# Performance work log

Hardware: AMD Instinct MI355X
Metric: run time of the kernel (lower is better)

Reference implementation:

```python
import jax, jax.numpy as jnp
import numpy as np

B, D, T, H, E = 4, 1024, 2048, 16, 64  # batch, dim, seq_len, n_heads, hidden_dim (H*E == D)


def setup_inputs() -> dict:
    key = jax.random.key(0)
    ks = jax.random.split(key, 6)
    x = jax.random.normal(ks[0], (B, D, T), dtype=jnp.float32)            # (b, e, t) layout
    Wp = jax.random.normal(ks[1], (H, E, D), dtype=jnp.float32) / np.sqrt(D)  # per-head proj weights
    bp = jax.random.normal(ks[2], (H, E), dtype=jnp.float32) * 0.01
    tw = jax.random.normal(ks[3], (H, T), dtype=jnp.float32) / np.sqrt(T)  # per-head Toeplitz kernel, tw[h,0]=diagonal
    Wo = jax.random.normal(ks[4], (D, D), dtype=jnp.float32) / np.sqrt(D)
    bo = jax.random.normal(ks[5], (D,), dtype=jnp.float32) * 0.01
    return {"x": x, "Wp": Wp, "bp": bp, "tw": tw, "Wo": Wo, "bo": bo}


def reference(x, Wp, bp, tw, Wo, bo):
    # x: (b, dim, t) -> (b, t, dim)
    xt = jnp.transpose(x, (0, 2, 1))
    # per-head projections: (b, h, e, t)
    proj = jnp.einsum('btd,hed->bhet', xt, Wp) + bp[None, :, :, None]
    # build per-head causal lower-triangular Toeplitz matrices: Tm[h, t, s] = tw[h, t-s] if s <= t else 0
    idx = jnp.arange(T)[:, None] - jnp.arange(T)[None, :]  # (t, s)
    Tm = jnp.where(idx >= 0, tw[:, jnp.clip(idx, 0)], 0.0)  # (h, t, s)
    # causal Toeplitz mixing along time per head
    mixed = jnp.einsum('hts,bhes->bhet', Tm, proj)          # (b, h, e, t)
    # concat heads on feature dim: (b, t, h*e) == (b, t, dim)
    cat = jnp.transpose(mixed, (0, 3, 1, 2)).reshape(B, T, H * E)
    out = cat @ Wo.T + bo                                   # out_proj: Linear(dim, dim)
    return jnp.transpose(out, (0, 2, 1))                    # back to (b, e, t)
```

## Files before the change

kernel.cpp:

```cpp
#include <hip/hip_runtime.h>
#include <cstdint>

#define NB 4
#define ND 1024
#define NT 2048
#define NH 16
#define NE 64
#define GLEN 2240
#define CAP 2312

typedef __bf16 bf16x8 __attribute__((ext_vector_type(8)));
typedef float f32x4 __attribute__((ext_vector_type(4)));
typedef unsigned short us8 __attribute__((ext_vector_type(8)));
typedef unsigned short us4 __attribute__((ext_vector_type(4)));

__device__ __forceinline__ unsigned short f2bf(float f) {
  unsigned u = __builtin_bit_cast(unsigned, f);
  return (unsigned short)((u + 0x7fffu + ((u >> 16) & 1u)) >> 16);
}

__device__ __forceinline__ void gload16(const void* g, void* l) {
  __builtin_amdgcn_global_load_lds(
      (const __attribute__((address_space(1))) void*)(uintptr_t)g,
      (__attribute__((address_space(3))) void*)(uintptr_t)l, 16, 0, 0);
}

__global__ void prep_kernel(const float* __restrict__ Wp, const float* __restrict__ Wo,
                            const float* __restrict__ tw,
                            unsigned short* __restrict__ WpB, unsigned short* __restrict__ WoB,
                            unsigned short* __restrict__ Gr8) {
  int idx = blockIdx.x * 256 + threadIdx.x;
  int stride = gridDim.x * 256;
  const int n4 = ND * ND / 4;
  for (int i = idx; i < n4; i += stride) {
    float4 v = ((const float4*)Wp)[i];
    us4 o = {f2bf(v.x), f2bf(v.y), f2bf(v.z), f2bf(v.w)};
    ((us4*)WpB)[i] = o;
  }
  for (int i = idx; i < n4; i += stride) {
    float4 v = ((const float4*)Wo)[i];
    us4 o = {f2bf(v.x), f2bf(v.y), f2bf(v.z), f2bf(v.w)};
    ((us4*)WoB)[i] = o;
  }
  for (int i = idx; i < NH * 8 * GLEN; i += stride) {
    int h = i / (8 * GLEN);
    int rem = i - h * 8 * GLEN;
    int r = rem / GLEN;
    int c = rem - r * GLEN;
    int src = c + r;
    Gr8[i] = (src <= NT - 1) ? f2bf(tw[h * NT + (NT - 1) - src]) : (unsigned short)0;
  }
}

__global__ __launch_bounds__(256) void transpose_cast(const float* __restrict__ x,
                                                      unsigned short* __restrict__ xT) {
  __shared__ float tile[64][65];
  const int c = threadIdx.x & 15, r = threadIdx.x >> 4;
  const int t0 = blockIdx.x * 64, d0 = blockIdx.y * 64, b = blockIdx.z;
  const float* xb = x + (long)b * ND * NT;
#pragma unroll
  for (int k = 0; k < 4; ++k) {
    float4 v = *(const float4*)&xb[(long)(d0 + r + 16 * k) * NT + t0 + 4 * c];
    tile[r + 16 * k][4 * c + 0] = v.x;
    tile[r + 16 * k][4 * c + 1] = v.y;
    tile[r + 16 * k][4 * c + 2] = v.z;
    tile[r + 16 * k][4 * c + 3] = v.w;
  }
  __syncthreads();
  unsigned short* xTb = xT + (long)b * NT * ND;
#pragma unroll
  for (int k = 0; k < 4; ++k) {
    int t = r + 16 * k;
    us4 o = {f2bf(tile[4 * c + 0][t]), f2bf(tile[4 * c + 1][t]), f2bf(tile[4 * c + 2][t]),
             f2bf(tile[4 * c + 3][t])};
    *(us4*)&xTb[(long)(t0 + t) * ND + d0 + 4 * c] = o;
  }
}

template <bool OUT_BF16>
__global__ __launch_bounds__(512, 2) void gemm_bt(const unsigned short* __restrict__ A,
                                                  const unsigned short* __restrict__ Bt,
                                                  const float* __restrict__ bias,
                                                  void* __restrict__ Cb, long strideB,
                                                  long strideC) {
  const int N = 2048, K = 1024;
  __shared__ __align__(16) unsigned short As[3][128 * 64];
  __shared__ __align__(16) unsigned short Bs[3][256 * 64];
  const int tid = threadIdx.x;
  const int lane = tid & 63;
  const int wid = tid >> 6;
  const int wm = (wid & 1) * 64, wn = (wid >> 1) * 64;
  const int m0 = blockIdx.y * 128, n0 = blockIdx.x * 256;
  const unsigned short* Bb = Bt + (long)blockIdx.z * strideB;
  const int mlo = lane & 15, q = lane >> 4, m7 = mlo & 7;

  const int r0 = tid >> 3;
  const int xblk = (tid & 7) ^ (r0 & 7);
  const unsigned short* aSrc = A + (long)(m0 + r0) * K + xblk * 8;
  const unsigned short* bSrc = Bb + (long)(n0 + r0) * K + xblk * 8;

  auto stage0 = [&](int buf, int t) {
    gload16(aSrc + t * 64, &As[buf][tid * 8]);
    gload16(aSrc + 64 * (long)K + t * 64, &As[buf][(512 + tid) * 8]);
    gload16(bSrc + t * 64, &Bs[buf][tid * 8]);
  };
  auto stage1 = [&](int buf, int t) {
    gload16(bSrc + 64 * (long)K + t * 64, &Bs[buf][(512 + tid) * 8]);
    gload16(bSrc + 128 * (long)K + t * 64, &Bs[buf][(1024 + tid) * 8]);
    gload16(bSrc + 192 * (long)K + t * 64, &Bs[buf][(1536 + tid) * 8]);
  };

  f32x4 acc[4][4] = {};
  stage0(0, 0);
  stage1(0, 0);
  stage0(1, 1);
  stage1(1, 1);

#pragma unroll
  for (int t = 0; t < 16; ++t) {
    const int buf = t % 3;
    if (t < 15)
      asm volatile("s_waitcnt vmcnt(6) lgkmcnt(0)" ::: "memory");
    else
      asm volatile("s_waitcnt vmcnt(0) lgkmcnt(0)" ::: "memory");
    __builtin_amdgcn_s_barrier();
#pragma unroll
    for (int ks = 0; ks < 2; ++ks) {
      bf16x8 av[4], bv[4];
      const int xb8 = ((4 * ks + q) ^ m7) * 8;
#pragma unroll
      for (int i = 0; i < 4; ++i) {
        av[i] = __builtin_bit_cast(bf16x8, *(const us8*)&As[buf][(wm + i * 16 + mlo) * 64 + xb8]);
        bv[i] = __builtin_bit_cast(bf16x8, *(const us8*)&Bs[buf][(wn + i * 16 + mlo) * 64 + xb8]);
      }
      if (t + 2 < 16) {
        if (ks == 0)
          stage0((t + 2) % 3, t + 2);
        else
          stage1((t + 2) % 3, t + 2);
      }
      __builtin_amdgcn_s_setprio(1);
#pragma unroll
      for (int i = 0; i < 4; ++i)
#pragma unroll
        for (int j = 0; j < 4; ++j)
          acc[i][j] = __builtin_amdgcn_mfma_f32_16x16x32_bf16(av[i], bv[j], acc[i][j], 0, 0, 0);
      __builtin_amdgcn_s_setprio(0);
    }
  }

#pragma unroll
  for (int i = 0; i < 4; ++i)
#pragma unroll
    for (int j = 0; j < 4; ++j)
#pragma unroll
      for (int r = 0; r < 4; ++r) {
        int gr = m0 + wm + i * 16 + q * 4 + r;
        int gc = n0 + wn + j * 16 + mlo;
        float v = acc[i][j][r] + bias[gr];
        if (OUT_BF16)
          ((unsigned short*)Cb)[(long)blockIdx.z * strideC + (long)gr * N + gc] = f2bf(v);
        else
          ((float*)Cb)[(long)blockIdx.z * strideC + (long)gr * N + gc] = v;
      }
}

__global__ __launch_bounds__(256, 2) void toeplitz(const unsigned short* __restrict__ proj,
                                                   const unsigned short* __restrict__ Gr8,
                                                   unsigned short* __restrict__ mixedT) {
  __shared__ __align__(16) unsigned short Ls[8 * CAP];
  __shared__ __align__(16) unsigned short Bs[2][2][64 * 32];
  const int tid = threadIdx.x, lane = tid & 63, w = tid >> 6;
  const int j = blockIdx.x, h = blockIdx.y, bz = blockIdx.z;
  const int mlo = lane & 15, q = lane >> 4;
  const int wt = (w >> 1) * 64, we = (w & 1) * 32;
  const int t0L = (15 - j) * 128, t0S = j * 128;

  const int delta = (NT - 128) - t0L;
  const int MUSE = t0L + 256;
#pragma unroll 1
  for (int r = 0; r < 8; ++r) {
    int rr = (r + delta) & 7;
    int off8 = r + delta - rr;
    const unsigned short* src = Gr8 + (long)(h * 8 + rr) * GLEN + off8;
    unsigned short* dst = &Ls[r * CAP];
    for (int mc = tid; mc * 8 < MUSE; mc += 256) gload16(src + mc * 8, dst + mc * 8);
  }

  const int rA = (7 - mlo) & 7;
  const int eRow = tid >> 2, kCol = (tid & 3) * 8;
  const unsigned short* bsrc = proj + ((long)bz * ND + h * 64 + eRow) * NT + kCol;

#pragma unroll 1
  for (int p = 0; p < 2; ++p) {
    const int t0p = p ? t0S : t0L;
    const int kend = t0p + 128;
    const unsigned short* lA = &Ls[rA * CAP + (127 - wt - mlo - rA) + q * 8 + (t0L - t0p)];
    gload16(bsrc, &Bs[0][0][tid * 8]);
    gload16(bsrc + 32, &Bs[0][1][tid * 8]);
    __syncthreads();
    bf16x8 ap0 = __builtin_bit_cast(bf16x8, *(const us8*)(lA - 32));
    bf16x8 ap1 = __builtin_bit_cast(bf16x8, *(const us8*)(lA - 48));
    f32x4 acc[4][2] = {};

    auto sub = [&](int bf, int hh, int s) {
      bf16x8 a0 = __builtin_bit_cast(bf16x8, *(const us8*)(lA + s));
      bf16x8 a1 = __builtin_bit_cast(bf16x8, *(const us8*)(lA + s - 16));
      bf16x8 b0 = __builtin_bit_cast(bf16x8, *(const us8*)&Bs[bf][hh][(we + mlo) * 32 + q * 8]);
      bf16x8 b1 =
          __builtin_bit_cast(bf16x8, *(const us8*)&Bs[bf][hh][(we + 16 + mlo) * 32 + q * 8]);
      acc[0][0] = __builtin_amdgcn_mfma_f32_16x16x32_bf16(a0, b0, acc[0][0], 0, 0, 0);
      acc[0][1] = __builtin_amdgcn_mfma_f32_16x16x32_bf16(a0, b1, acc[0][1], 0, 0, 0);
      acc[1][0] = __builtin_amdgcn_mfma_f32_16x16x32_bf16(a1, b0, acc[1][0], 0, 0, 0);
      acc[1][1] = __builtin_amdgcn_mfma_f32_16x16x32_bf16(a1, b1, acc[1][1], 0, 0, 0);
      acc[2][0] = __builtin_amdgcn_mfma_f32_16x16x32_bf16(ap0, b0, acc[2][0], 0, 0, 0);
      acc[2][1] = __builtin_amdgcn_mfma_f32_16x16x32_bf16(ap0, b1, acc[2][1], 0, 0, 0);
      acc[3][0] = __builtin_amdgcn_mfma_f32_16x16x32_bf16(ap1, b0, acc[3][0], 0, 0, 0);
      acc[3][1] = __builtin_amdgcn_mfma_f32_16x16x32_bf16(ap1, b1, acc[3][1], 0, 0, 0);
      ap0 = a0;
      ap1 = a1;
    };

#pragma unroll 1
    for (int s0 = 0; s0 < kend; s0 += 128) {
      gload16(bsrc + s0 + 64, &Bs[1][0][tid * 8]);
      gload16(bsrc + s0 + 96, &Bs[1][1][tid * 8]);
      sub(0, 0, s0);
      sub(0, 1, s0 + 32);
      __syncthreads();
      if (s0 + 128 < kend) {
        gload16(bsrc + s0 + 128, &Bs[0][0][tid * 8]);
        gload16(bsrc + s0 + 160, &Bs[0][1][tid * 8]);
      }
      sub(1, 0, s0 + 64);
      sub(1, 1, s0 + 96);
      __syncthreads();
    }
#pragma unroll
    for (int i = 0; i < 4; ++i)
#pragma unroll
      for (int jj = 0; jj < 2; ++jj)
#pragma unroll
        for (int rr = 0; rr < 4; ++rr) {
          int t = t0p + wt + i * 16 + q * 4 + rr;
          int e = we + jj * 16 + mlo;
          mixedT[((long)bz * NT + t) * ND + h * 64 + e] = f2bf(acc[i][jj][rr]);
        }
  }
}

extern "C" void kernel_launch(void* const* d_in, const int* in_sizes, int n_in, void* d_out,
                              int out_size, void* d_ws, size_t ws_size, hipStream_t stream) {
  const float* x = (const float*)d_in[0];
  const float* Wp = (const float*)d_in[1];
  const float* bp = (const float*)d_in[2];
  const float* tw = (const float*)d_in[3];
  const float* Wo = (const float*)d_in[4];
  const float* bo = (const float*)d_in[5];
  float* out = (float*)d_out;

  char* ws = (char*)d_ws;
  unsigned short* xT = (unsigned short*)(ws);
  unsigned short* proj = (unsigned short*)(ws + (16ull << 20));
  unsigned short* WpB = (unsigned short*)(ws + (32ull << 20));
  unsigned short* WoB = (unsigned short*)(ws + (34ull << 20));
  unsigned short* Gr8 = (unsigned short*)(ws + (36ull << 20));

  prep_kernel<<<dim3(1024), 256, 0, stream>>>(Wp, Wo, tw, WpB, WoB, Gr8);
  transpose_cast<<<dim3(NT / 64, ND / 64, NB), 256, 0, stream>>>(x, xT);
  gemm_bt<true><<<dim3(8, 8, NB), 512, 0, stream>>>(WpB, xT, bp, proj, (long)NT * ND,
                                                    (long)ND * NT);
  toeplitz<<<dim3(8, NH, NB), 256, 0, stream>>>(proj, Gr8, xT);
  gemm_bt<false><<<dim3(8, 8, NB), 512, 0, stream>>>(WoB, xT, bo, out, (long)NT * ND,
                                                     (long)ND * NT);
}
```

Baseline: 158.2 us.

## Merge Toeplitz passes into one 4-stage async pipeline with one barrier per chunk

The two causal passes of the Toeplitz kernel now run as one flat loop over 64-wide K chunks. A 4-deep LDS ring is kept filled three chunks ahead, and explicit vmcnt waits replace the paired __syncthreads per 128 columns. This removes the pipeline drain and refill between the long and short passes, halves the barriers, and raises MFMA priority with s_setprio. In exchange the kernel uses twice the B-tile LDS, which may hurt occupancy, and relies on hand-counted waitcnt values being correct.

Measured after the change: 159.7 us. Within noise of the previous version (+1.0%).

```diff
diff --git a/kernel.cpp b/kernel.cpp
--- a/kernel.cpp
+++ b/kernel.cpp
@@ -169,7 +169,7 @@
                                                    const unsigned short* __restrict__ Gr8,
                                                    unsigned short* __restrict__ mixedT) {
   __shared__ __align__(16) unsigned short Ls[8 * CAP];
-  __shared__ __align__(16) unsigned short Bs[2][2][64 * 32];
+  __shared__ __align__(16) unsigned short Bs[4][2][64 * 32];
   const int tid = threadIdx.x, lane = tid & 63, w = tid >> 6;
   const int j = blockIdx.x, h = blockIdx.y, bz = blockIdx.z;
   const int mlo = lane & 15, q = lane >> 4;
@@ -191,61 +191,84 @@
   const int eRow = tid >> 2, kCol = (tid & 3) * 8;
   const unsigned short* bsrc = proj + ((long)bz * ND + h * 64 + eRow) * NT + kCol;
 
+  const int nc0 = 2 * (16 - j);
+  const int NCT = 34;
+  const unsigned short* lA0 = &Ls[rA * CAP + (127 - wt - mlo - rA) + q * 8];
+  const unsigned short* lA1 = lA0 + (t0L - t0S);
+
+  auto stage = [&](int g) {
+    int c = (g < nc0) ? g : g - nc0;
+    gload16(bsrc + c * 64, &Bs[g & 3][0][tid * 8]);
+    gload16(bsrc + c * 64 + 32, &Bs[g & 3][1][tid * 8]);
+  };
+
+  stage(0);
+  stage(1);
+  stage(2);
+
+  f32x4 acc[4][2];
+  bf16x8 ap0 = {}, ap1 = {};
+  const unsigned short* lA = lA0;
+
+  auto sub = [&](int bf, int hh, int s) {
+    bf16x8 a0 = __builtin_bit_cast(bf16x8, *(const us8*)(lA + s));
+    bf16x8 a1 = __builtin_bit_cast(bf16x8, *(const us8*)(lA + s - 16));
+    bf16x8 b0 = __builtin_bit_cast(bf16x8, *(const us8*)&Bs[bf][hh][(we + mlo) * 32 + q * 8]);
+    bf16x8 b1 = __builtin_bit_cast(bf16x8, *(const us8*)&Bs[bf][hh][(we + 16 + mlo) * 32 + q * 8]);
+    acc[0][0] = __builtin_amdgcn_mfma_f32_16x16x32_bf16(a0, b0, acc[0][0], 0, 0, 0);
+    acc[0][1] = __builtin_amdgcn_mfma_f32_16x16x32_bf16(a0, b1, acc[0][1], 0, 0, 0);
+    acc[1][0] = __builtin_amdgcn_mfma_f32_16x16x32_bf16(a1, b0, acc[1][0], 0, 0, 0);
+    acc[1][1] = __builtin_amdgcn_mfma_f32_16x16x32_bf16(a1, b1, acc[1][1], 0, 0, 0);
+    acc[2][0] = __builtin_amdgcn_mfma_f32_16x16x32_bf16(ap0, b0, acc[2][0], 0, 0, 0);
+    acc[2][1] = __builtin_amdgcn_mfma_f32_16x16x32_bf16(ap0, b1, acc[2][1], 0, 0, 0);
+    acc[3][0] = __builtin_amdgcn_mfma_f32_16x16x32_bf16(ap1, b0, acc[3][0], 0, 0, 0);
+    acc[3][1] = __builtin_amdgcn_mfma_f32_16x16x32_bf16(ap1, b1, acc[3][1], 0, 0, 0);
+    ap0 = a0;
+    ap1 = a1;
+  };
+
 #pragma unroll 1
-  for (int p = 0; p < 2; ++p) {
-    const int t0p = p ? t0S : t0L;
-    const int kend = t0p + 128;
-    const unsigned short* lA = &Ls[rA * CAP + (127 - wt - mlo - rA) + q * 8 + (t0L - t0p)];
-    gload16(bsrc, &Bs[0][0][tid * 8]);
-    gload16(bsrc + 32, &Bs[0][1][tid * 8]);
-    __syncthreads();
-    bf16x8 ap0 = __builtin_bit_cast(bf16x8, *(const us8*)(lA - 32));
-    bf16x8 ap1 = __builtin_bit_cast(bf16x8, *(const us8*)(lA - 48));
-    f32x4 acc[4][2] = {};
-
-    auto sub = [&](int bf, int hh, int s) {
-      bf16x8 a0 = __builtin_bit_cast(bf16x8, *(const us8*)(lA + s));
-      bf16x8 a1 = __builtin_bit_cast(bf16x8, *(const us8*)(lA + s - 16));
-      bf16x8 b0 = __builtin_bit_cast(bf16x8, *(const us8*)&Bs[bf][hh][(we + mlo) * 32 + q * 8]);
-      bf16x8 b1 =
-          __builtin_bit_cast(bf16x8, *(const us8*)&Bs[bf][hh][(we + 16 + mlo) * 32 + q * 8]);
-      acc[0][0] = __builtin_amdgcn_mfma_f32_16x16x32_bf16(a0, b0, acc[0][0], 0, 0, 0);
-      acc[0][1] = __builtin_amdgcn_mfma_f32_16x16x32_bf16(a0, b1, acc[0][1], 0, 0, 0);
-      acc[1][0] = __builtin_amdgcn_mfma_f32_16x16x32_bf16(a1, b0, acc[1][0], 0, 0, 0);
-      acc[1][1] = __builtin_amdgcn_mfma_f32_16x16x32_bf16(a1, b1, acc[1][1], 0, 0, 0);
-      acc[2][0] = __builtin_amdgcn_mfma_f32_16x16x32_bf16(ap0, b0, acc[2][0], 0, 0, 0);
-      acc[2][1] = __builtin_amdgcn_mfma_f32_16x16x32_bf16(ap0, b1, acc[2][1], 0, 0, 0);
-      acc[3][0] = __builtin_amdgcn_mfma_f32_16x16x32_bf16(ap1, b0, acc[3][0], 0, 0, 0);
-      acc[3][1] = __builtin_amdgcn_mfma_f32_16x16x32_bf16(ap1, b1, acc[3][1], 0, 0, 0);
-      ap0 = a0;
-      ap1 = a1;
-    };
-
-#pragma unroll 1
-    for (int s0 = 0; s0 < kend; s0 += 128) {
-      gload16(bsrc + s0 + 64, &Bs[1][0][tid * 8]);
-      gload16(bsrc + s0 + 96, &Bs[1][1][tid * 8]);
-      sub(0, 0, s0);
-      sub(0, 1, s0 + 32);
-      __syncthreads();
-      if (s0 + 128 < kend) {
-        gload16(bsrc + s0 + 128, &Bs[0][0][tid * 8]);
-        gload16(bsrc + s0 + 160, &Bs[0][1][tid * 8]);
-      }
-      sub(1, 0, s0 + 64);
-      sub(1, 1, s0 + 96);
-      __syncthreads();
+  for (int g = 0; g < NCT; ++g) {
+    if (g + 2 < NCT)
+      asm volatile("s_waitcnt vmcnt(4) lgkmcnt(0)" ::: "memory");
+    else if (g + 1 < NCT)
+      asm volatile("s_waitcnt vmcnt(2) lgkmcnt(0)" ::: "memory");
+    else
+      asm volatile("s_waitcnt vmcnt(0) lgkmcnt(0)" ::: "memory");
+    __builtin_amdgcn_s_barrier();
+    if (g + 3 < NCT) stage(g + 3);
+
+    const int pass = (g >= nc0) ? 1 : 0;
+    const int c = pass ? g - nc0 : g;
+    if (c == 0) {
+      lA = pass ? lA1 : lA0;
+      ap0 = __builtin_bit_cast(bf16x8, *(const us8*)(lA - 32));
+      ap1 = __builtin_bit_cast(bf16x8, *(const us8*)(lA - 48));
+#pragma unroll
+      for (int i = 0; i < 4; ++i)
+#pragma unroll
+        for (int jj = 0; jj < 2; ++jj) acc[i][jj] = f32x4{0.f, 0.f, 0.f, 0.f};
     }
-#pragma unroll
-    for (int i = 0; i < 4; ++i)
-#pragma unroll
-      for (int jj = 0; jj < 2; ++jj)
-#pragma unroll
-        for (int rr = 0; rr < 4; ++rr) {
-          int t = t0p + wt + i * 16 + q * 4 + rr;
-          int e = we + jj * 16 + mlo;
-          mixedT[((long)bz * NT + t) * ND + h * 64 + e] = f2bf(acc[i][jj][rr]);
-        }
+    const int buf = g & 3;
+    const int s0 = c * 64;
+    __builtin_amdgcn_s_setprio(1);
+    sub(buf, 0, s0);
+    sub(buf, 1, s0 + 32);
+    __builtin_amdgcn_s_setprio(0);
+
+    if ((!pass && g == nc0 - 1) || g == NCT - 1) {
+      const int t0p = pass ? t0S : t0L;
+#pragma unroll
+      for (int i = 0; i < 4; ++i)
+#pragma unroll
+        for (int jj = 0; jj < 2; ++jj)
+#pragma unroll
+          for (int rr = 0; rr < 4; ++rr) {
+            int t = t0p + wt + i * 16 + q * 4 + rr;
+            int e = we + jj * 16 + mlo;
+            mixedT[((long)bz * NT + t) * ND + h * 64 + e] = f2bf(acc[i][jj][rr]);
+          }
+    }
   }
 }
 
```
